# Kernel optimization log

Hardware: AMD Instinct MI355X
Metric: run time of the kernel (lower is better)

## Reference

```python
import jax, jax.numpy as jnp
import numpy as np

N_USERS, N_ITEMS, DIM, LAYERS, NNZ = 50000, 50000, 128, 2, 1600000
N = N_USERS + N_ITEMS


def setup_inputs() -> dict:
    key = jax.random.key(0)
    ks = jax.random.split(key, 8)
    adj_row = jax.random.randint(ks[0], (NNZ,), 0, N, dtype=jnp.int32)
    adj_col = jax.random.randint(ks[1], (NNZ,), 0, N, dtype=jnp.int32)
    # normalized-adjacency-like small positive values (~1/avg_degree)
    adj_vals = jax.random.uniform(ks[2], (NNZ,), dtype=jnp.float32) * 0.0625
    emb = jax.random.normal(ks[3], (N, DIM), dtype=jnp.float32) * 0.1  # xavier-ish
    W1_w = jax.random.normal(ks[4], (LAYERS, DIM, DIM), dtype=jnp.float32) * (1.0 / np.sqrt(DIM))
    W1_b = jnp.zeros((LAYERS, DIM), dtype=jnp.float32)
    W2_w = jax.random.normal(ks[5], (LAYERS, DIM, DIM), dtype=jnp.float32) * (1.0 / np.sqrt(DIM))
    W2_b = jnp.zeros((LAYERS, DIM), dtype=jnp.float32)
    return {"adj_row": adj_row, "adj_col": adj_col, "adj_vals": adj_vals,
            "emb": emb, "W1_w": W1_w, "W1_b": W1_b, "W2_w": W2_w, "W2_b": W2_b}


def reference(adj_row, adj_col, adj_vals, emb, W1_w, W1_b, W2_w, W2_b):
    n = emb.shape[0]
    x = emb
    embs = [x]
    for k in range(W1_w.shape[0]):
        # SpMM: side = norm_adj @ x  (COO gather + segment-sum)
        side = jax.ops.segment_sum(adj_vals[:, None] * x[adj_col], adj_row, num_segments=n)
        # two dense transforms (torch Linear: y = x @ W.T + b), fused add + leaky_relu
        x = jax.nn.leaky_relu((side + x) @ W1_w[k].T + W1_b[k]
                              + (side * x) @ W2_w[k].T + W2_b[k],
                              negative_slope=0.01)
        # dropout is identity in eval mode; L2-normalize rows (F.normalize eps=1e-12)
        x = x / jnp.maximum(jnp.linalg.norm(x, axis=1, keepdims=True), 1e-12)
        embs.append(x)
    return jnp.concatenate(embs, axis=1)  # [N, dim*(layers+1)]
```

## Files before the change

### kernel.cpp

```cpp
#include <hip/hip_runtime.h>
#include <stdint.h>

#define N_NODES 100000
#define NPAD    100032
#define DIM 128
#define NNZ_E 1600000
#define SCAN_TILE 2048
#define N_TILES ((N_NODES + SCAN_TILE - 1) / SCAN_TILE)

typedef float f32x4  __attribute__((ext_vector_type(4)));
typedef short bf16x8 __attribute__((ext_vector_type(8)));

union B8 { uint4 q; unsigned u[4]; bf16x8 v; };

__device__ __forceinline__ unsigned short f2bs(float f) {
    unsigned u = __builtin_bit_cast(unsigned, f);
    u = (u + 0x7fffu + ((u >> 16) & 1u)) >> 16;
    return (unsigned short)u;
}
__device__ __forceinline__ unsigned cvtpk(float lo, float hi) {
    unsigned r;
    asm("v_cvt_pk_bf16_f32 %0, %1, %2" : "=v"(r) : "v"(lo), "v"(hi));
    return r;
}
#define UNPK(u32, flo, fhi) { flo = __builtin_bit_cast(float, (unsigned)((u32) << 16)); \
                              fhi = __builtin_bit_cast(float, (unsigned)((u32) & 0xffff0000u)); }

__global__ __launch_bounds__(256) void copy_emb_kernel(
    const float* __restrict__ emb, float* __restrict__ out,
    unsigned* __restrict__ xbuf)
{
    int tid = blockIdx.x * 256 + threadIdx.x;
    int n = tid >> 5, c = tid & 31;
    if (n < N_NODES) {
        float4 v = ((const float4*)emb)[tid];
        *((float4*)(out + (size_t)n * 384) + c) = v;
        ((uint2*)xbuf)[(size_t)n * 32 + c] = make_uint2(cvtpk(v.x, v.y), cvtpk(v.z, v.w));
    } else {
        ((uint2*)xbuf)[(size_t)n * 32 + c] = make_uint2(0u, 0u);
    }
}

__global__ __launch_bounds__(256) void prep_kernel(
    const float* __restrict__ W1, const float* __restrict__ W2,
    unsigned* __restrict__ w1b, unsigned* __restrict__ w2b,
    int* __restrict__ cnt)
{
    int tid = blockIdx.x * 256 + threadIdx.x;
    if (tid < 8192) {
        float4 a = ((const float4*)W1)[tid];
        float4 b = ((const float4*)W2)[tid];
        ((uint2*)w1b)[tid] = make_uint2(cvtpk(a.x, a.y), cvtpk(a.z, a.w));
        ((uint2*)w2b)[tid] = make_uint2(cvtpk(b.x, b.y), cvtpk(b.z, b.w));
    }
    if (tid < 25000) ((uint4*)cnt)[tid] = make_uint4(0u, 0u, 0u, 0u);
}

__global__ __launch_bounds__(256) void hist_kernel(
    const int* __restrict__ rows, int* __restrict__ cnt)
{
    int e = blockIdx.x * 256 + threadIdx.x;
    atomicAdd(&cnt[rows[e]], 1);
}

__global__ __launch_bounds__(256) void scan_pass_a(
    const int* __restrict__ cnt, int* __restrict__ tile_sums)
{
    __shared__ int sdata[256];
    int base = blockIdx.x * SCAN_TILE + threadIdx.x * 8;
    int s = 0;
    #pragma unroll
    for (int q = 0; q < 8; ++q) {
        int i = base + q;
        s += (i < N_NODES) ? cnt[i] : 0;
    }
    sdata[threadIdx.x] = s;
    __syncthreads();
    for (int off = 128; off >= 1; off >>= 1) {
        if (threadIdx.x < off) sdata[threadIdx.x] += sdata[threadIdx.x + off];
        __syncthreads();
    }
    if (threadIdx.x == 0) tile_sums[blockIdx.x] = sdata[0];
}

__global__ void scan_pass_b(int* __restrict__ tile_sums)
{
    int lane = threadIdx.x;
    int v = (lane < N_TILES) ? tile_sums[lane] : 0;
    #pragma unroll
    for (int off = 1; off < 64; off <<= 1) {
        int u = __shfl_up(v, off);
        if (lane >= off) v += u;
    }
    int ex = __shfl_up(v, 1);
    if (lane == 0) ex = 0;
    if (lane < N_TILES) tile_sums[lane] = ex;
}

__global__ __launch_bounds__(256) void scan_pass_c(
    const int* __restrict__ cnt, const int* __restrict__ tile_offs,
    int* __restrict__ row_ptr)
{
    __shared__ int spart[256];
    int t = threadIdx.x;
    int base = blockIdx.x * SCAN_TILE + t * 8;
    int loc[8];
    int s = 0;
    #pragma unroll
    for (int q = 0; q < 8; ++q) {
        int i = base + q;
        int c = (i < N_NODES) ? cnt[i] : 0;
        loc[q] = s; s += c;
    }
    spart[t] = s;
    __syncthreads();
    for (int off = 1; off < 256; off <<= 1) {
        int v = (t >= off) ? spart[t - off] : 0;
        __syncthreads();
        spart[t] += v;
        __syncthreads();
    }
    int exoff = tile_offs[blockIdx.x] + spart[t] - s;
    #pragma unroll
    for (int q = 0; q < 8; ++q) {
        int i = base + q;
        if (i <= N_NODES) row_ptr[i] = exoff + loc[q];
    }
}

__global__ __launch_bounds__(256) void scatter_kernel(
    const int* __restrict__ rows, const int* __restrict__ cols,
    const float* __restrict__ vals, const int* __restrict__ row_ptr,
    int* __restrict__ cnt, int2* __restrict__ edges)
{
    int e = blockIdx.x * 256 + threadIdx.x;
    int r = rows[e];
    int pos = row_ptr[r] + atomicSub(&cnt[r], 1) - 1;
    edges[pos] = make_int2(cols[e], __float_as_int(vals[e]));
}

__global__ __launch_bounds__(256) void spmm_gather_bf16(
    const int* __restrict__ row_ptr, const int2* __restrict__ edges,
    const unsigned* __restrict__ xb, unsigned* __restrict__ sideb)
{
    int row  = blockIdx.x * 4 + (threadIdx.x >> 6);
    int lane = threadIdx.x & 63;
    if (row >= N_NODES) {
        sideb[(size_t)row * 64 + lane] = 0u;
        return;
    }
    int beg = row_ptr[row], end = row_ptr[row + 1];
    float ax = 0.f, ay = 0.f;
    int i = beg;
    int nfull = (end - beg) & ~7;
    if (nfull) {
        int2 e[8];
        #pragma unroll
        for (int u = 0; u < 8; ++u) e[u] = edges[i + u];
        for (int g = 8; g < nfull; g += 8) {
            int2 f[8];
            #pragma unroll
            for (int u = 0; u < 8; ++u) f[u] = edges[i + 8 + u];
            #pragma unroll
            for (int u = 0; u < 8; ++u) {
                unsigned xu = xb[(size_t)e[u].x * 64 + lane];
                float v = __int_as_float(e[u].y), lo, hi;
                UNPK(xu, lo, hi); ax += v * lo; ay += v * hi;
            }
            #pragma unroll
            for (int u = 0; u < 8; ++u) e[u] = f[u];
            i += 8;
        }
        #pragma unroll
        for (int u = 0; u < 8; ++u) {
            unsigned xu = xb[(size_t)e[u].x * 64 + lane];
            float v = __int_as_float(e[u].y), lo, hi;
            UNPK(xu, lo, hi); ax += v * lo; ay += v * hi;
        }
        i += 8;
    }
    for (; i < end; ++i) {
        int2 e = edges[i];
        unsigned xu = xb[(size_t)e.x * 64 + lane];
        float v = __int_as_float(e.y), lo, hi;
        UNPK(xu, lo, hi); ax += v * lo; ay += v * hi;
    }
    sideb[(size_t)row * 64 + lane] = cvtpk(ax, ay);
}

__global__ __launch_bounds__(256) void dense_mfma_kernel(
    const unsigned* __restrict__ sideb, unsigned* __restrict__ xbuf,
    const unsigned* __restrict__ w1b, const unsigned* __restrict__ w2b,
    const float* __restrict__ b1, const float* __restrict__ b2,
    float* __restrict__ out, int outoff, int write_x)
{
    __shared__ __align__(16) unsigned sA1[64 * 64];
    __shared__ __align__(16) unsigned sA2[64 * 64];
    __shared__ float sPart[256];

    const int t = threadIdx.x;
    const int wave = t >> 6, lane = t & 63;
    const int q = lane >> 4, r = lane & 15;
    const int colbase = wave * 32;
    const int base = blockIdx.x * 64;

    bf16x8 Wf[2][2][4];
    {
        const uint4* w1p = (const uint4*)w1b;
        const uint4* w2p = (const uint4*)w2b;
        #pragma unroll
        for (int nt = 0; nt < 2; ++nt) {
            int j = colbase + nt * 16 + r;
            #pragma unroll
            for (int kk = 0; kk < 4; ++kk) {
                B8 a, b;
                a.q = w1p[j * 16 + kk * 4 + q];
                b.q = w2p[j * 16 + kk * 4 + q];
                Wf[0][nt][kk] = a.v;
                Wf[1][nt][kk] = b.v;
            }
        }
    }
    const float bias0 = b1[colbase + r]      + b2[colbase + r];
    const float bias1 = b1[colbase + 16 + r] + b2[colbase + 16 + r];

    {
        const int n = t >> 2, seg = t & 3;
        const uint4* sp = (const uint4*)sideb + ((size_t)(base + n)) * 16 + seg * 4;
        const uint4* xp = (const uint4*)xbuf  + ((size_t)(base + n)) * 16 + seg * 4;
        unsigned* d1 = sA1 + n * 64;
        unsigned* d2 = sA2 + n * 64;
        const int sw = n & 7, seg4 = seg * 4;
        #pragma unroll
        for (int j = 0; j < 4; ++j) {
            uint4 sv = sp[j];
            uint4 xv = xp[j];
            float s0,s1,s2,s3,s4,s5,s6,s7;
            float x0,x1,x2,x3,x4,x5,x6,x7;
            UNPK(sv.x, s0, s1); UNPK(sv.y, s2, s3);
            UNPK(sv.z, s4, s5); UNPK(sv.w, s6, s7);
            UNPK(xv.x, x0, x1); UNPK(xv.y, x2, x3);
            UNPK(xv.z, x4, x5); UNPK(xv.w, x6, x7);
            uint4 a1q, a2q;
            a1q.x = cvtpk(s0 + x0, s1 + x1);
            a1q.y = cvtpk(s2 + x2, s3 + x3);
            a1q.z = cvtpk(s4 + x4, s5 + x5);
            a1q.w = cvtpk(s6 + x6, s7 + x7);
            a2q.x = cvtpk(s0 * x0, s1 * x1);
            a2q.y = cvtpk(s2 * x2, s3 * x3);
            a2q.z = cvtpk(s4 * x4, s5 * x5);
            a2q.w = cvtpk(s6 * x6, s7 * x7);
            int slot = (seg4 + j) ^ sw;
            *(uint4*)(d1 + slot * 4) = a1q;
            *(uint4*)(d2 + slot * 4) = a2q;
        }
    }
    __syncthreads();

    f32x4 acc[4][2];
    #pragma unroll
    for (int mt = 0; mt < 4; ++mt) {
        acc[mt][0] = (f32x4){0.f, 0.f, 0.f, 0.f};
        acc[mt][1] = (f32x4){0.f, 0.f, 0.f, 0.f};
    }
    int slotk[4];
    {
        const int sw = r & 7;
        #pragma unroll
        for (int kk = 0; kk < 4; ++kk) slotk[kk] = ((kk * 4 + q) ^ sw) * 4;
    }
    #pragma unroll
    for (int mt = 0; mt < 4; ++mt) {
        const unsigned* p1 = sA1 + (mt * 16 + r) * 64;
        const unsigned* p2 = sA2 + (mt * 16 + r) * 64;
        #pragma unroll
        for (int kk = 0; kk < 4; ++kk) {
            B8 a1, a2;
            a1.q = *(const uint4*)(p1 + slotk[kk]);
            a2.q = *(const uint4*)(p2 + slotk[kk]);
            acc[mt][0] = __builtin_amdgcn_mfma_f32_16x16x32_bf16(a1.v, Wf[0][0][kk], acc[mt][0], 0, 0, 0);
            acc[mt][0] = __builtin_amdgcn_mfma_f32_16x16x32_bf16(a2.v, Wf[1][0][kk], acc[mt][0], 0, 0, 0);
            acc[mt][1] = __builtin_amdgcn_mfma_f32_16x16x32_bf16(a1.v, Wf[0][1][kk], acc[mt][1], 0, 0, 0);
            acc[mt][1] = __builtin_amdgcn_mfma_f32_16x16x32_bf16(a2.v, Wf[1][1][kk], acc[mt][1], 0, 0, 0);
        }
    }

    #pragma unroll
    for (int mt = 0; mt < 4; ++mt) {
        #pragma unroll
        for (int i = 0; i < 4; ++i) {
            float y0 = acc[mt][0][i] + bias0; y0 = (y0 >= 0.f) ? y0 : 0.01f * y0;
            float y1 = acc[mt][1][i] + bias1; y1 = (y1 >= 0.f) ? y1 : 0.01f * y1;
            acc[mt][0][i] = y0; acc[mt][1][i] = y1;
            float s = y0 * y0 + y1 * y1;
            s += __shfl_xor(s, 1); s += __shfl_xor(s, 2);
            s += __shfl_xor(s, 4); s += __shfl_xor(s, 8);
            if (r == 0) sPart[wave * 64 + mt * 16 + q * 4 + i] = s;
        }
    }
    __syncthreads();

    #pragma unroll
    for (int mt = 0; mt < 4; ++mt) {
        #pragma unroll
        for (int i = 0; i < 4; ++i) {
            int nl = mt * 16 + q * 4 + i;
            float tot = sPart[nl] + sPart[64 + nl] + sPart[128 + nl] + sPart[192 + nl];
            float inv = 1.0f / fmaxf(sqrtf(tot), 1e-12f);
            int node = base + nl;
            if (node < N_NODES) {
                float y0 = acc[mt][0][i] * inv;
                float y1 = acc[mt][1][i] * inv;
                out[(size_t)node * 384 + outoff + colbase + r]      = y0;
                out[(size_t)node * 384 + outoff + colbase + 16 + r] = y1;
                if (write_x) {
                    ((unsigned short*)xbuf)[(size_t)node * 128 + colbase + r]      = f2bs(y0);
                    ((unsigned short*)xbuf)[(size_t)node * 128 + colbase + 16 + r] = f2bs(y1);
                }
            }
        }
    }
}

extern "C" void kernel_launch(void* const* d_in, const int* in_sizes, int n_in,
                              void* d_out, int out_size, void* d_ws, size_t ws_size,
                              hipStream_t stream)
{
    const int*   adj_row  = (const int*)d_in[0];
    const int*   adj_col  = (const int*)d_in[1];
    const float* adj_vals = (const float*)d_in[2];
    const float* emb      = (const float*)d_in[3];
    const float* W1_w     = (const float*)d_in[4];
    const float* W1_b     = (const float*)d_in[5];
    const float* W2_w     = (const float*)d_in[6];
    const float* W2_b     = (const float*)d_in[7];
    float* out = (float*)d_out;

    uint8_t* w = (uint8_t*)d_ws;
    unsigned* xbuf    = (unsigned*)(w);
    unsigned* sideb   = (unsigned*)(w + 25608192);
    int2*     edges   = (int2*)    (w + 51216384);
    unsigned* w1b     = (unsigned*)(w + 64016384);
    unsigned* w2b     = (unsigned*)(w + 64081920);
    int*      row_ptr = (int*)     (w + 64147456);
    int*      cnt     = (int*)     (w + 64547472);
    int*      tsums   = (int*)     (w + 64947488);

    prep_kernel<<<128, 256, 0, stream>>>(W1_w, W2_w, w1b, w2b, cnt);
    copy_emb_kernel<<<NPAD * 32 / 256, 256, 0, stream>>>(emb, out, xbuf);

    hist_kernel<<<NNZ_E / 256, 256, 0, stream>>>(adj_row, cnt);
    scan_pass_a<<<N_TILES, 256, 0, stream>>>(cnt, tsums);
    scan_pass_b<<<1, 64, 0, stream>>>(tsums);
    scan_pass_c<<<N_TILES, 256, 0, stream>>>(cnt, tsums, row_ptr);
    scatter_kernel<<<NNZ_E / 256, 256, 0, stream>>>(
        adj_row, adj_col, adj_vals, row_ptr, cnt, edges);

    for (int k = 0; k < 2; ++k) {
        spmm_gather_bf16<<<NPAD / 4, 256, 0, stream>>>(row_ptr, edges, xbuf, sideb);
        dense_mfma_kernel<<<NPAD / 64, 256, 0, stream>>>(
            sideb, xbuf, w1b + k * 8192, w2b + k * 8192,
            W1_b + k * DIM, W2_b + k * DIM,
            out, DIM * (k + 1), (k == 0) ? 1 : 0);
    }
}
```

Baseline: 577.6 us.

## Fuse SpMM gather into dense MFMA layer kernel with ping-pong x buffers

Merges the per-row SpMM gather and the dense MFMA transform into one kernel per layer. Each 16-thread group gathers whole 16-byte bf16 rows per edge, using shuffles to broadcast edge indices, and writes the combined operands straight into shared memory. This removes the side buffer round trip through global memory and one launch per layer. It adds separate input and output x buffers so the in-place update stays safe. The trade-off is that gather latency is now spread over fewer waves per row, since each block handles 64 nodes with 16 lanes per node, and load imbalance between nodes can stall the MFMA phase.

```diff
diff --git a/kernel.cpp b/kernel.cpp
--- a/kernel.cpp
+++ b/kernel.cpp
@@ -139,57 +139,9 @@
     edges[pos] = make_int2(cols[e], __float_as_int(vals[e]));
 }
 
-__global__ __launch_bounds__(256) void spmm_gather_bf16(
+__global__ __launch_bounds__(256) void fused_layer_kernel(
     const int* __restrict__ row_ptr, const int2* __restrict__ edges,
-    const unsigned* __restrict__ xb, unsigned* __restrict__ sideb)
-{
-    int row  = blockIdx.x * 4 + (threadIdx.x >> 6);
-    int lane = threadIdx.x & 63;
-    if (row >= N_NODES) {
-        sideb[(size_t)row * 64 + lane] = 0u;
-        return;
-    }
-    int beg = row_ptr[row], end = row_ptr[row + 1];
-    float ax = 0.f, ay = 0.f;
-    int i = beg;
-    int nfull = (end - beg) & ~7;
-    if (nfull) {
-        int2 e[8];
-        #pragma unroll
-        for (int u = 0; u < 8; ++u) e[u] = edges[i + u];
-        for (int g = 8; g < nfull; g += 8) {
-            int2 f[8];
-            #pragma unroll
-            for (int u = 0; u < 8; ++u) f[u] = edges[i + 8 + u];
-            #pragma unroll
-            for (int u = 0; u < 8; ++u) {
-                unsigned xu = xb[(size_t)e[u].x * 64 + lane];
-                float v = __int_as_float(e[u].y), lo, hi;
-                UNPK(xu, lo, hi); ax += v * lo; ay += v * hi;
-            }
-            #pragma unroll
-            for (int u = 0; u < 8; ++u) e[u] = f[u];
-            i += 8;
-        }
-        #pragma unroll
-        for (int u = 0; u < 8; ++u) {
-            unsigned xu = xb[(size_t)e[u].x * 64 + lane];
-            float v = __int_as_float(e[u].y), lo, hi;
-            UNPK(xu, lo, hi); ax += v * lo; ay += v * hi;
-        }
-        i += 8;
-    }
-    for (; i < end; ++i) {
-        int2 e = edges[i];
-        unsigned xu = xb[(size_t)e.x * 64 + lane];
-        float v = __int_as_float(e.y), lo, hi;
-        UNPK(xu, lo, hi); ax += v * lo; ay += v * hi;
-    }
-    sideb[(size_t)row * 64 + lane] = cvtpk(ax, ay);
-}
-
-__global__ __launch_bounds__(256) void dense_mfma_kernel(
-    const unsigned* __restrict__ sideb, unsigned* __restrict__ xbuf,
+    const unsigned* __restrict__ xin, unsigned* __restrict__ xout,
     const unsigned* __restrict__ w1b, const unsigned* __restrict__ w2b,
     const float* __restrict__ b1, const float* __restrict__ b2,
     float* __restrict__ out, int outoff, int write_x)
@@ -201,8 +153,61 @@
     const int t = threadIdx.x;
     const int wave = t >> 6, lane = t & 63;
     const int q = lane >> 4, r = lane & 15;
+    const int G = t >> 4;
+    const int l = t & 15;
     const int colbase = wave * 32;
     const int base = blockIdx.x * 64;
+    const uint4* xin4 = (const uint4*)xin;
+
+    for (int nn = 0; nn < 4; ++nn) {
+        const int n = G * 4 + nn;
+        const int node = base + n;
+        float s0=0.f,s1=0.f,s2=0.f,s3=0.f,s4=0.f,s5=0.f,s6=0.f,s7=0.f;
+        float x0=0.f,x1=0.f,x2=0.f,x3=0.f,x4=0.f,x5=0.f,x6=0.f,x7=0.f;
+        if (node < N_NODES) {
+            const int beg = row_ptr[node], end = row_ptr[node + 1];
+            const int cnt = end - beg;
+            const int nb = cnt >> 4;
+            #define GEDGE(u) { \
+                int col = __shfl(e.x, (u), 16); \
+                float v = __int_as_float(__shfl(e.y, (u), 16)); \
+                uint4 xv = xin4[(size_t)col * 16 + l]; \
+                float lo, hi; \
+                UNPK(xv.x, lo, hi); s0 += v * lo; s1 += v * hi; \
+                UNPK(xv.y, lo, hi); s2 += v * lo; s3 += v * hi; \
+                UNPK(xv.z, lo, hi); s4 += v * lo; s5 += v * hi; \
+                UNPK(xv.w, lo, hi); s6 += v * lo; s7 += v * hi; }
+            for (int b = 0; b < nb; ++b) {
+                int2 e = edges[beg + b * 16 + l];
+                GEDGE(0)  GEDGE(1)  GEDGE(2)  GEDGE(3)
+                GEDGE(4)  GEDGE(5)  GEDGE(6)  GEDGE(7)
+                GEDGE(8)  GEDGE(9)  GEDGE(10) GEDGE(11)
+                GEDGE(12) GEDGE(13) GEDGE(14) GEDGE(15)
+            }
+            const int rem = cnt & 15;
+            if (rem) {
+                int idx = beg + nb * 16 + l;
+                int2 e = edges[idx < end ? idx : end - 1];
+                for (int u = 0; u < rem; ++u) GEDGE(u)
+            }
+            #undef GEDGE
+            uint4 xv = xin4[(size_t)node * 16 + l];
+            UNPK(xv.x, x0, x1); UNPK(xv.y, x2, x3);
+            UNPK(xv.z, x4, x5); UNPK(xv.w, x6, x7);
+        }
+        uint4 a1q, a2q;
+        a1q.x = cvtpk(s0 + x0, s1 + x1);
+        a1q.y = cvtpk(s2 + x2, s3 + x3);
+        a1q.z = cvtpk(s4 + x4, s5 + x5);
+        a1q.w = cvtpk(s6 + x6, s7 + x7);
+        a2q.x = cvtpk(s0 * x0, s1 * x1);
+        a2q.y = cvtpk(s2 * x2, s3 * x3);
+        a2q.z = cvtpk(s4 * x4, s5 * x5);
+        a2q.w = cvtpk(s6 * x6, s7 * x7);
+        const int slot = l ^ (n & 7);
+        *(uint4*)(sA1 + n * 64 + slot * 4) = a1q;
+        *(uint4*)(sA2 + n * 64 + slot * 4) = a2q;
+    }
 
     bf16x8 Wf[2][2][4];
     {
@@ -223,38 +228,6 @@
     }
     const float bias0 = b1[colbase + r]      + b2[colbase + r];
     const float bias1 = b1[colbase + 16 + r] + b2[colbase + 16 + r];
-
-    {
-        const int n = t >> 2, seg = t & 3;
-        const uint4* sp = (const uint4*)sideb + ((size_t)(base + n)) * 16 + seg * 4;
-        const uint4* xp = (const uint4*)xbuf  + ((size_t)(base + n)) * 16 + seg * 4;
-        unsigned* d1 = sA1 + n * 64;
-        unsigned* d2 = sA2 + n * 64;
-        const int sw = n & 7, seg4 = seg * 4;
-        #pragma unroll
-        for (int j = 0; j < 4; ++j) {
-            uint4 sv = sp[j];
-            uint4 xv = xp[j];
-            float s0,s1,s2,s3,s4,s5,s6,s7;
-            float x0,x1,x2,x3,x4,x5,x6,x7;
-            UNPK(sv.x, s0, s1); UNPK(sv.y, s2, s3);
-            UNPK(sv.z, s4, s5); UNPK(sv.w, s6, s7);
-            UNPK(xv.x, x0, x1); UNPK(xv.y, x2, x3);
-            UNPK(xv.z, x4, x5); UNPK(xv.w, x6, x7);
-            uint4 a1q, a2q;
-            a1q.x = cvtpk(s0 + x0, s1 + x1);
-            a1q.y = cvtpk(s2 + x2, s3 + x3);
-            a1q.z = cvtpk(s4 + x4, s5 + x5);
-            a1q.w = cvtpk(s6 + x6, s7 + x7);
-            a2q.x = cvtpk(s0 * x0, s1 * x1);
-            a2q.y = cvtpk(s2 * x2, s3 * x3);
-            a2q.z = cvtpk(s4 * x4, s5 * x5);
-            a2q.w = cvtpk(s6 * x6, s7 * x7);
-            int slot = (seg4 + j) ^ sw;
-            *(uint4*)(d1 + slot * 4) = a1q;
-            *(uint4*)(d2 + slot * 4) = a2q;
-        }
-    }
     __syncthreads();
 
     f32x4 acc[4][2];
@@ -314,8 +287,8 @@
                 out[(size_t)node * 384 + outoff + colbase + r]      = y0;
                 out[(size_t)node * 384 + outoff + colbase + 16 + r] = y1;
                 if (write_x) {
-                    ((unsigned short*)xbuf)[(size_t)node * 128 + colbase + r]      = f2bs(y0);
-                    ((unsigned short*)xbuf)[(size_t)node * 128 + colbase + 16 + r] = f2bs(y1);
+                    ((unsigned short*)xout)[(size_t)node * 128 + colbase + r]      = f2bs(y0);
+                    ((unsigned short*)xout)[(size_t)node * 128 + colbase + 16 + r] = f2bs(y1);
                 }
             }
         }
@@ -337,8 +310,8 @@
     float* out = (float*)d_out;
 
     uint8_t* w = (uint8_t*)d_ws;
-    unsigned* xbuf    = (unsigned*)(w);
-    unsigned* sideb   = (unsigned*)(w + 25608192);
+    unsigned* xA      = (unsigned*)(w);
+    unsigned* xB      = (unsigned*)(w + 25608192);
     int2*     edges   = (int2*)    (w + 51216384);
     unsigned* w1b     = (unsigned*)(w + 64016384);
     unsigned* w2b     = (unsigned*)(w + 64081920);
@@ -347,7 +320,7 @@
     int*      tsums   = (int*)     (w + 64947488);
 
     prep_kernel<<<128, 256, 0, stream>>>(W1_w, W2_w, w1b, w2b, cnt);
-    copy_emb_kernel<<<NPAD * 32 / 256, 256, 0, stream>>>(emb, out, xbuf);
+    copy_emb_kernel<<<NPAD * 32 / 256, 256, 0, stream>>>(emb, out, xA);
 
     hist_kernel<<<NNZ_E / 256, 256, 0, stream>>>(adj_row, cnt);
     scan_pass_a<<<N_TILES, 256, 0, stream>>>(cnt, tsums);
@@ -356,11 +329,9 @@
     scatter_kernel<<<NNZ_E / 256, 256, 0, stream>>>(
         adj_row, adj_col, adj_vals, row_ptr, cnt, edges);
 
-    for (int k = 0; k < 2; ++k) {
-        spmm_gather_bf16<<<NPAD / 4, 256, 0, stream>>>(row_ptr, edges, xbuf, sideb);
-        dense_mfma_kernel<<<NPAD / 64, 256, 0, stream>>>(
-            sideb, xbuf, w1b + k * 8192, w2b + k * 8192,
-            W1_b + k * DIM, W2_b + k * DIM,
-            out, DIM * (k + 1), (k == 0) ? 1 : 0);
-    }
-}
+    fused_layer_kernel<<<NPAD / 64, 256, 0, stream>>>(
+        row_ptr, edges, xA, xB, w1b, w2b, W1_b, W2_b, out, DIM, 1);
+    fused_layer_kernel<<<NPAD / 64, 256, 0, stream>>>(
+        row_ptr, edges, xB, xB, w1b + 8192, w2b + 8192,
+        W1_b + DIM, W2_b + DIM, out, 2 * DIM, 0);
+}
```

New measurement: 693.3 us. +20.0%, slower.

## Slice bf16 embeddings into column-sliced layout so SpMM gathers stay cache-resident

Applied to the files above, without the earlier changes.

Stores the bf16 node features as 8 column slices of 16 features each. The SpMM is now split so each block handles one slice for 32 rows, with 8 lanes per row sharing edge loads through shuffles. The intent is that each slice's gather working set (about 3.2 MB) fits in L2, which should cut random-access DRAM traffic. In exchange, edges are re-read 8 times, reads are narrower, ping-pong x buffers are introduced, and the dense kernel must read and write the sliced layout.

```diff
diff --git a/kernel.cpp b/kernel.cpp
--- a/kernel.cpp
+++ b/kernel.cpp
@@ -8,6 +8,7 @@
 #define SCAN_TILE 2048
 #define N_TILES ((N_NODES + SCAN_TILE - 1) / SCAN_TILE)
 
+
 typedef float f32x4  __attribute__((ext_vector_type(4)));
 typedef short bf16x8 __attribute__((ext_vector_type(8)));
 
@@ -32,12 +33,14 @@
 {
     int tid = blockIdx.x * 256 + threadIdx.x;
     int n = tid >> 5, c = tid & 31;
+    int s = c >> 2, m = c & 3;
+    uint2* dst = (uint2*)xbuf + ((size_t)s * NPAD + n) * 4 + m;
     if (n < N_NODES) {
         float4 v = ((const float4*)emb)[tid];
         *((float4*)(out + (size_t)n * 384) + c) = v;
-        ((uint2*)xbuf)[(size_t)n * 32 + c] = make_uint2(cvtpk(v.x, v.y), cvtpk(v.z, v.w));
+        *dst = make_uint2(cvtpk(v.x, v.y), cvtpk(v.z, v.w));
     } else {
-        ((uint2*)xbuf)[(size_t)n * 32 + c] = make_uint2(0u, 0u);
+        *dst = make_uint2(0u, 0u);
     }
 }
 
@@ -139,57 +142,65 @@
     edges[pos] = make_int2(cols[e], __float_as_int(vals[e]));
 }
 
-__global__ __launch_bounds__(256) void spmm_gather_bf16(
+__global__ __launch_bounds__(256) void spmm_slice(
     const int* __restrict__ row_ptr, const int2* __restrict__ edges,
-    const unsigned* __restrict__ xb, unsigned* __restrict__ sideb)
-{
-    int row  = blockIdx.x * 4 + (threadIdx.x >> 6);
-    int lane = threadIdx.x & 63;
-    if (row >= N_NODES) {
-        sideb[(size_t)row * 64 + lane] = 0u;
-        return;
-    }
-    int beg = row_ptr[row], end = row_ptr[row + 1];
-    float ax = 0.f, ay = 0.f;
+    const unsigned* __restrict__ xs, unsigned* __restrict__ sides)
+{
+    const int s = blockIdx.x & 7;
+    const int g = blockIdx.x >> 3;
+    const int t = threadIdx.x;
+    const int l = t & 7;
+    const int row = g * 32 + (t >> 3);
+    unsigned* sp = sides + ((size_t)s * NPAD + row) * 8 + l;
+    if (row >= N_NODES) { *sp = 0u; return; }
+
+    const unsigned* xsl = xs + (size_t)s * NPAD * 8 + l;
+    const long long* ed = (const long long*)edges;
+    const int beg = row_ptr[row], end = row_ptr[row + 1];
+    float a0 = 0.f, a1 = 0.f;
     int i = beg;
-    int nfull = (end - beg) & ~7;
+    const int nfull = (end - beg) & ~7;
+
+    #define CHUNK8(E) { \
+        int clo = (int)(E); \
+        int chi = (int)((unsigned long long)(E) >> 32); \
+        int cols[8]; float vs[8]; unsigned gv[8]; \
+        _Pragma("unroll") \
+        for (int u = 0; u < 8; ++u) { \
+            cols[u] = __shfl(clo, u, 8); \
+            vs[u]   = __int_as_float(__shfl(chi, u, 8)); \
+        } \
+        _Pragma("unroll") \
+        for (int u = 0; u < 8; ++u) gv[u] = xsl[(size_t)cols[u] * 8]; \
+        _Pragma("unroll") \
+        for (int u = 0; u < 8; ++u) { \
+            float lo, hi; UNPK(gv[u], lo, hi); \
+            a0 += vs[u] * lo; a1 += vs[u] * hi; \
+        } }
+
     if (nfull) {
-        int2 e[8];
-        #pragma unroll
-        for (int u = 0; u < 8; ++u) e[u] = edges[i + u];
-        for (int g = 8; g < nfull; g += 8) {
-            int2 f[8];
-            #pragma unroll
-            for (int u = 0; u < 8; ++u) f[u] = edges[i + 8 + u];
-            #pragma unroll
-            for (int u = 0; u < 8; ++u) {
-                unsigned xu = xb[(size_t)e[u].x * 64 + lane];
-                float v = __int_as_float(e[u].y), lo, hi;
-                UNPK(xu, lo, hi); ax += v * lo; ay += v * hi;
-            }
-            #pragma unroll
-            for (int u = 0; u < 8; ++u) e[u] = f[u];
-            i += 8;
-        }
-        #pragma unroll
-        for (int u = 0; u < 8; ++u) {
-            unsigned xu = xb[(size_t)e[u].x * 64 + lane];
-            float v = __int_as_float(e[u].y), lo, hi;
-            UNPK(xu, lo, hi); ax += v * lo; ay += v * hi;
-        }
+        long long e = __builtin_nontemporal_load(ed + i + l);
+        for (int c = 8; c < nfull; c += 8) {
+            long long f = __builtin_nontemporal_load(ed + i + 8 + l);
+            CHUNK8(e)
+            e = f; i += 8;
+        }
+        CHUNK8(e)
         i += 8;
     }
+    #undef CHUNK8
     for (; i < end; ++i) {
-        int2 e = edges[i];
-        unsigned xu = xb[(size_t)e.x * 64 + lane];
-        float v = __int_as_float(e.y), lo, hi;
-        UNPK(xu, lo, hi); ax += v * lo; ay += v * hi;
-    }
-    sideb[(size_t)row * 64 + lane] = cvtpk(ax, ay);
+        int2 d = edges[i];
+        unsigned xv = xsl[(size_t)d.x * 8];
+        float v = __int_as_float(d.y), lo, hi;
+        UNPK(xv, lo, hi); a0 += v * lo; a1 += v * hi;
+    }
+    __builtin_nontemporal_store(cvtpk(a0, a1), sp);
 }
 
 __global__ __launch_bounds__(256) void dense_mfma_kernel(
-    const unsigned* __restrict__ sideb, unsigned* __restrict__ xbuf,
+    const unsigned* __restrict__ sideb, const unsigned* __restrict__ xbuf,
+    unsigned* __restrict__ xout,
     const unsigned* __restrict__ w1b, const unsigned* __restrict__ w2b,
     const float* __restrict__ b1, const float* __restrict__ b2,
     float* __restrict__ out, int outoff, int write_x)
@@ -225,16 +236,19 @@
     const float bias1 = b1[colbase + 16 + r] + b2[colbase + 16 + r];
 
     {
-        const int n = t >> 2, seg = t & 3;
-        const uint4* sp = (const uint4*)sideb + ((size_t)(base + n)) * 16 + seg * 4;
-        const uint4* xp = (const uint4*)xbuf  + ((size_t)(base + n)) * 16 + seg * 4;
+        const int n = t & 63, seg = t >> 6;
+        const size_t node = (size_t)(base + n);
+        const uint4* sq = (const uint4*)sideb;
+        const uint4* xq = (const uint4*)xbuf;
         unsigned* d1 = sA1 + n * 64;
         unsigned* d2 = sA2 + n * 64;
-        const int sw = n & 7, seg4 = seg * 4;
+        const int sw = n & 7;
         #pragma unroll
         for (int j = 0; j < 4; ++j) {
-            uint4 sv = sp[j];
-            uint4 xv = xp[j];
+            const int sl = 2 * seg + (j >> 1), h = j & 1;
+            const size_t idx = ((size_t)sl * NPAD + node) * 2 + h;
+            uint4 sv = sq[idx];
+            uint4 xv = xq[idx];
             float s0,s1,s2,s3,s4,s5,s6,s7;
             float x0,x1,x2,x3,x4,x5,x6,x7;
             UNPK(sv.x, s0, s1); UNPK(sv.y, s2, s3);
@@ -250,7 +264,7 @@
             a2q.y = cvtpk(s2 * x2, s3 * x3);
             a2q.z = cvtpk(s4 * x4, s5 * x5);
             a2q.w = cvtpk(s6 * x6, s7 * x7);
-            int slot = (seg4 + j) ^ sw;
+            int slot = (seg * 4 + j) ^ sw;
             *(uint4*)(d1 + slot * 4) = a1q;
             *(uint4*)(d2 + slot * 4) = a2q;
         }
@@ -314,8 +328,8 @@
                 out[(size_t)node * 384 + outoff + colbase + r]      = y0;
                 out[(size_t)node * 384 + outoff + colbase + 16 + r] = y1;
                 if (write_x) {
-                    ((unsigned short*)xbuf)[(size_t)node * 128 + colbase + r]      = f2bs(y0);
-                    ((unsigned short*)xbuf)[(size_t)node * 128 + colbase + 16 + r] = f2bs(y1);
+                    ((unsigned short*)xout)[((size_t)(wave * 2)     * NPAD + node) * 16 + r] = f2bs(y0);
+                    ((unsigned short*)xout)[((size_t)(wave * 2 + 1) * NPAD + node) * 16 + r] = f2bs(y1);
                 }
             }
         }
@@ -337,17 +351,22 @@
     float* out = (float*)d_out;
 
     uint8_t* w = (uint8_t*)d_ws;
-    unsigned* xbuf    = (unsigned*)(w);
-    unsigned* sideb   = (unsigned*)(w + 25608192);
+    unsigned* xA      = (unsigned*)(w);
+    unsigned* xB      = (unsigned*)(w + 25608192);
+    unsigned* sideb   = xB;
     int2*     edges   = (int2*)    (w + 51216384);
     unsigned* w1b     = (unsigned*)(w + 64016384);
     unsigned* w2b     = (unsigned*)(w + 64081920);
     int*      row_ptr = (int*)     (w + 64147456);
     int*      cnt     = (int*)     (w + 64547472);
     int*      tsums   = (int*)     (w + 64947488);
+    (void)sideb;
+
+    unsigned* xS = (unsigned*)(w + 64947504 + 256);
+    xS = (unsigned*)(w + ((64947488 + 49 * 4 + 255) & ~255ull));
 
     prep_kernel<<<128, 256, 0, stream>>>(W1_w, W2_w, w1b, w2b, cnt);
-    copy_emb_kernel<<<NPAD * 32 / 256, 256, 0, stream>>>(emb, out, xbuf);
+    copy_emb_kernel<<<NPAD * 32 / 256, 256, 0, stream>>>(emb, out, xA);
 
     hist_kernel<<<NNZ_E / 256, 256, 0, stream>>>(adj_row, cnt);
     scan_pass_a<<<N_TILES, 256, 0, stream>>>(cnt, tsums);
@@ -356,11 +375,11 @@
     scatter_kernel<<<NNZ_E / 256, 256, 0, stream>>>(
         adj_row, adj_col, adj_vals, row_ptr, cnt, edges);
 
-    for (int k = 0; k < 2; ++k) {
-        spmm_gather_bf16<<<NPAD / 4, 256, 0, stream>>>(row_ptr, edges, xbuf, sideb);
-        dense_mfma_kernel<<<NPAD / 64, 256, 0, stream>>>(
-            sideb, xbuf, w1b + k * 8192, w2b + k * 8192,
-            W1_b + k * DIM, W2_b + k * DIM,
-            out, DIM * (k + 1), (k == 0) ? 1 : 0);
-    }
-}
+    spmm_slice<<<(NPAD / 32) * 8, 256, 0, stream>>>(row_ptr, edges, xA, xS);
+    dense_mfma_kernel<<<NPAD / 64, 256, 0, stream>>>(
+        xS, xA, xB, w1b, w2b, W1_b, W2_b, out, DIM, 1);
+    spmm_slice<<<(NPAD / 32) * 8, 256, 0, stream>>>(row_ptr, edges, xB, xS);
+    dense_mfma_kernel<<<NPAD / 64, 256, 0, stream>>>(
+        xS, xB, xB, w1b + 8192, w2b + 8192,
+        W1_b + DIM, W2_b + DIM, out, 2 * DIM, 0);
+}
```

Result: slower. 733.0 us (+26.9%).
